# Kernel optimization log

Measured on AMD Instinct MI355X. Metric: run time of the kernel, lower is better.

Reference implementation:

```python
import math
import jax, jax.numpy as jnp
import numpy as np

B, T, D = 2, 1024, 768          # batch, seq, hidden
H = 12                          # attention heads
DH_ATT = D // H
PH, NK, TOPK, DHK = 4, 256, 32, 128  # pkm heads, num product keys, topk, key dim
DQ = PH * DHK * 2               # pkm query projection width
EPS = 1e-5


def _ln(x, g, b):
    m = jnp.mean(x, -1, keepdims=True)
    v = jnp.var(x, -1, keepdims=True)
    return (x - m) * jax.lax.rsqrt(v + EPS) * g + b


def setup_inputs() -> dict:
    key = jax.random.key(0)
    k = jax.random.split(key, 8)
    n = lambda i, s, sc=0.02: jax.random.normal(k[i], s, jnp.float32) * sc
    z = lambda s: jnp.zeros(s, jnp.float32)
    o = lambda s: jnp.ones(s, jnp.float32)
    return {
        "hidden_states": jax.random.normal(k[0], (B, T, D), jnp.float32),
        "wq": n(1, (D, D)), "bq": z((D,)),
        "wk": n(2, (D, D)), "bk": z((D,)),
        "wv": n(3, (D, D)), "bv": z((D,)),
        "wo": n(4, (D, D)), "bo": z((D,)),
        "ln1_g": o((D,)), "ln1_b": z((D,)),
        "ln2_g": o((D,)), "ln2_b": z((D,)),
        "pkm_wq": n(5, (D, DQ)),
        "bn_g": o((DQ,)), "bn_b": z((DQ,)),
        "pkm_keys": n(6, (PH, NK, 2, DHK), 1.0 / math.sqrt(DHK)),
        "pkm_values": n(7, (NK * NK, D), 1.0 / math.sqrt(D)),
    }


def reference(hidden_states, wq, bq, wk, bk, wv, bv, wo, bo,
              ln1_g, ln1_b, ln2_g, ln2_b,
              pkm_wq, bn_g, bn_b, pkm_keys, pkm_values):
    x = hidden_states
    # ---- pre-norm self-attention + residual ----
    h = _ln(x, ln1_g, ln1_b)
    q = (h @ wq + bq).reshape(B, T, H, DH_ATT)
    k = (h @ wk + bk).reshape(B, T, H, DH_ATT)
    v = (h @ wv + bv).reshape(B, T, H, DH_ATT)
    scores = jnp.einsum('bqhd,bkhd->bhqk', q, k) / math.sqrt(DH_ATT)
    probs = jax.nn.softmax(scores, axis=-1)
    attn_out = jnp.einsum('bhqk,bkhd->bqhd', probs, v).reshape(B, T, D) @ wo + bo
    x = x + attn_out
    # ---- pre-norm PKM + residual ----
    h = _ln(x, ln2_g, ln2_b)
    qf = (h @ pkm_wq).reshape(B * T, DQ)
    # BatchNorm1d over tokens (training-mode batch stats)
    mu = jnp.mean(qf, 0)
    var = jnp.var(qf, 0)
    qn = (qf - mu) * jax.lax.rsqrt(var + EPS) * bn_g + bn_b
    # split into the two sub-key query halves: [2, n, PH, DHK]
    qh = jnp.stack(jnp.split(qn, 2, axis=-1)).reshape(2, B * T, PH, DHK)
    # distances against both sub-key codebooks: [n, PH, 2, NK]
    dots = jnp.einsum('pnhd,hkpd->nhpk', qh, pkm_keys)
    s, idx = jax.lax.top_k(dots, TOPK)                       # [n, PH, 2, TOPK]
    all_s = (s[:, :, 0, :, None] + s[:, :, 1, None, :]).reshape(B * T, PH, TOPK * TOPK)
    all_i = (idx[:, :, 0, :, None] * NK + idx[:, :, 1, None, :]).reshape(B * T, PH, TOPK * TOPK)
    fs, fpos = jax.lax.top_k(all_s, TOPK)                    # [n, PH, TOPK]
    vi = jnp.take_along_axis(all_i, fpos, axis=-1)           # cartesian indices
    attn = jax.nn.softmax(fs, axis=-1)
    # EmbeddingBag(mode='sum') with per_sample_weights: gather + weighted sum over PH*TOPK
    pkm_out = jnp.einsum('nhk,nhkd->nd', attn, pkm_values[vi]).reshape(B, T, D)
    return x + pkm_out
```

## Files before the change

kernel.cpp:

```cpp
#include <hip/hip_runtime.h>
#include <hip/hip_bf16.h>

#define B_  2
#define T_  1024
#define D_  768
#define H_  12
#define NT  2048
#define DQ_ 1024
#define PH_ 4
#define NK_ 256
#define TK_ 32
#define DHK_ 128
#define QKVLD 2304
#define CVHALF 25165824L
#define NKEYS (PH_ * NK_ * 2 * DHK_)
#define PREPBLKS 3584

typedef __attribute__((ext_vector_type(8))) short bf16x8;
typedef __attribute__((ext_vector_type(4))) float f32x4;
typedef __attribute__((ext_vector_type(2))) float f32x2;

static __device__ __forceinline__ unsigned short f2bf(float f) {
    union { float f; unsigned u; } c; c.f = f;
    unsigned r = (c.u + 0x7fffu + ((c.u >> 16) & 1u)) >> 16;
    return (unsigned short)r;
}

static __device__ __forceinline__ float bf2f(unsigned short s) {
    union { unsigned u; float f; } c; c.u = ((unsigned)s) << 16;
    return c.f;
}

__global__ __launch_bounds__(256)
void ln_kernel(const float* __restrict__ x, const float* __restrict__ g,
               const float* __restrict__ b, unsigned short* __restrict__ out,
               int nrows,
               const float* __restrict__ wq, const float* __restrict__ wk,
               const float* __restrict__ wv, const float* __restrict__ wo,
               const float* __restrict__ pwq, const float* __restrict__ keys,
               unsigned short* __restrict__ wqkvT, unsigned short* __restrict__ woT,
               unsigned short* __restrict__ pwqT, unsigned short* __restrict__ keyB) {
    int tid = threadIdx.x;
    if ((int)blockIdx.x >= nrows) {
        int tb = blockIdx.x - nrows;
        if (tb >= 3072) {
            long i = ((long)(tb - 3072) * 256 + tid) * 2;
            if (i + 1 < NKEYS + 1) { keyB[i] = f2bf(keys[i]); keyB[i + 1] = f2bf(keys[i + 1]); }
            return;
        }
        __shared__ float t[32][33];
        const float* W; unsigned short* Wt; int N, kx, ny;
        if (tb < 2304) {
            int z = tb / 576, rem = tb % 576;
            kx = rem % 24; ny = rem / 24; N = 768;
            if (z == 0)      { W = wq; Wt = wqkvT; }
            else if (z == 1) { W = wk; Wt = wqkvT + 589824; }
            else if (z == 2) { W = wv; Wt = wqkvT + 2 * 589824; }
            else             { W = wo; Wt = woT; }
        } else {
            int rem = tb - 2304;
            kx = rem % 24; ny = rem / 24; N = 1024;
            W = pwq; Wt = pwqT;
        }
        int k0 = kx * 32, n0 = ny * 32;
        int tx = tid & 31, ty = tid >> 5;
#pragma unroll
        for (int i = 0; i < 4; ++i)
            t[ty + 8 * i][tx] = W[(long)(k0 + ty + 8 * i) * N + n0 + tx];
        __syncthreads();
#pragma unroll
        for (int i = 0; i < 4; ++i)
            Wt[(long)(n0 + ty + 8 * i) * 768 + k0 + tx] = f2bf(t[tx][ty + 8 * i]);
        return;
    }

    int row = blockIdx.x;
    const float* xr = x + (long)row * D_;
    float v0 = xr[tid], v1 = xr[tid + 256], v2 = xr[tid + 512];
    float s = v0 + v1 + v2, ss = v0 * v0 + v1 * v1 + v2 * v2;
#pragma unroll
    for (int o = 1; o < 64; o <<= 1) { s += __shfl_xor(s, o); ss += __shfl_xor(ss, o); }
    __shared__ float ps[4], pss[4];
    int wid = tid >> 6, lane = tid & 63;
    if (lane == 0) { ps[wid] = s; pss[wid] = ss; }
    __syncthreads();
    s = ps[0] + ps[1] + ps[2] + ps[3];
    ss = pss[0] + pss[1] + pss[2] + pss[3];
    float mean = s * (1.f / D_);
    float var = ss * (1.f / D_) - mean * mean;
    float rs = rsqrtf(var + 1e-5f);
    unsigned short* orow = out + (long)row * D_;
    orow[tid]       = f2bf((v0 - mean) * rs * g[tid]       + b[tid]);
    orow[tid + 256] = f2bf((v1 - mean) * rs * g[tid + 256] + b[tid + 256]);
    orow[tid + 512] = f2bf((v2 - mean) * rs * g[tid + 512] + b[tid + 512]);
}

__global__ __launch_bounds__(256)
void gemm_kernel(const unsigned short* __restrict__ A, int lda,
                 const unsigned short* __restrict__ Bt, int ldb,
                 const float* __restrict__ bias,
                 const float* __restrict__ bias2,
                 const float* __restrict__ bias3,
                 const float* __restrict__ res,
                 float* __restrict__ outF,
                 unsigned short* __restrict__ outB,
                 int ldc, int K, int zmode,
                 const float* __restrict__ cvin,
                 unsigned char* __restrict__ cvout,
                 long cvbase, int cvy0) {
    if (cvin && (int)blockIdx.y >= cvy0) {
        long stride = (long)(gridDim.y - cvy0) * gridDim.x * 256 * 8;
        long idx = cvbase +
            ((long)((blockIdx.y - cvy0) * gridDim.x + blockIdx.x) * 256 + threadIdx.x) * 8;
        long end = cvbase + CVHALF;
#pragma unroll 2
        for (; idx < end; idx += stride) {
            f32x4 a = *(const f32x4*)(cvin + idx);
            f32x4 b = *(const f32x4*)(cvin + idx + 4);
            int lo = __builtin_amdgcn_cvt_pk_fp8_f32(a[0], a[1], 0, false);
            lo = __builtin_amdgcn_cvt_pk_fp8_f32(a[2], a[3], lo, true);
            int hi = __builtin_amdgcn_cvt_pk_fp8_f32(b[0], b[1], 0, false);
            hi = __builtin_amdgcn_cvt_pk_fp8_f32(b[2], b[3], hi, true);
            *(uint2*)(cvout + idx) = make_uint2((unsigned)lo, (unsigned)hi);
        }
        return;
    }
    if (zmode == 1) {
        int z = blockIdx.z, ph = z >> 1, half = z & 1;
        A    += half * 512 + ph * 128;
        Bt   += ph * 65536 + half * 128;
        if (outF) outF += ph * 512 + half * 256;
        if (outB) outB += ph * 512 + half * 256;
    }
    const int tid = threadIdx.x;
    const int w = tid >> 6, lane = tid & 63;
    const int ls = lane & 15, g = lane >> 4;
    const int m0 = blockIdx.x * 64, n0 = blockIdx.y * 64;

    __shared__ unsigned short As[64][40];
    __shared__ unsigned short Bs[64][40];

    f32x4 acc[4];
#pragma unroll
    for (int c = 0; c < 4; ++c) acc[c] = (f32x4){0.f, 0.f, 0.f, 0.f};

    const int lrow = tid >> 2, lseg = tid & 3;
    const unsigned short* gA = A + (long)(m0 + lrow) * lda + lseg * 8;
    const unsigned short* gB = Bt + (long)(n0 + lrow) * ldb + lseg * 8;

    for (int kt = 0; kt < K; kt += 32) {
        __syncthreads();
        *(int4*)&As[lrow][lseg * 8] = *(const int4*)(gA + kt);
        *(int4*)&Bs[lrow][lseg * 8] = *(const int4*)(gB + kt);
        __syncthreads();
        bf16x8 bfr = *(const bf16x8*)&Bs[w * 16 + ls][g * 8];
#pragma unroll
        for (int c = 0; c < 4; ++c) {
            bf16x8 afr = *(const bf16x8*)&As[c * 16 + ls][g * 8];
            acc[c] = __builtin_amdgcn_mfma_f32_16x16x32_bf16(afr, bfr, acc[c], 0, 0, 0);
        }
    }
#pragma unroll
    for (int c = 0; c < 4; ++c) {
#pragma unroll
        for (int r = 0; r < 4; ++r) {
            int row = m0 + c * 16 + g * 4 + r;
            int col = n0 + w * 16 + ls;
            float v = acc[c][r];
            if (bias) {
                const float* bp = bias; int cc = col;
                if (zmode == 2) {
                    int sel = col >= 1536 ? 2 : (col >= 768 ? 1 : 0);
                    bp = sel == 0 ? bias : (sel == 1 ? bias2 : bias3);
                    cc = col - sel * 768;
                }
                v += bp[cc];
            }
            long off = (long)row * ldc + col;
            if (res)  v += res[off];
            if (outF) outF[off] = v;
            if (outB) outB[off] = f2bf(v);
        }
    }
}

__global__ __launch_bounds__(512)
void attn_mfma_kernel(const unsigned short* __restrict__ qkv,
                      unsigned short* __restrict__ outg) {
    int bh = blockIdx.x, bb = bh / H_, hh = bh % H_;
    int q0 = blockIdx.y * 128;
    int tid = threadIdx.x, wv = tid >> 6, lane = tid & 63;
    int ls = lane & 15, g = lane >> 4;

    __shared__ unsigned short Klds[128 * 64];
    __shared__ unsigned short Vlds[64 * 128];
    __shared__ unsigned short Plds[8][16 * 128];

    const unsigned short* qrow = qkv + (long)(bb * T_ + q0 + wv * 16 + ls) * QKVLD + hh * 64 + g * 8;
    bf16x8 qf0 = *(const bf16x8*)qrow;
    bf16x8 qf1 = *(const bf16x8*)(qrow + 32);

    f32x4 o_acc[4];
#pragma unroll
    for (int nf = 0; nf < 4; ++nf) o_acc[nf] = (f32x4){0.f, 0.f, 0.f, 0.f};
    float mrun[4] = {-1e30f, -1e30f, -1e30f, -1e30f};
    float lrun[4] = {0.f, 0.f, 0.f, 0.f};

    char* pbase = (char*)&Plds[wv][0];
    const bool doK = tid < 256;
    const int t2 = tid & 255;
    const int d0 = (t2 & 7) * 8, kvq = t2 >> 3;

    bf16x8 streg[4];
    auto loadKV = [&](int kvb) {
        if (doK) {
#pragma unroll
            for (int i = 0; i < 4; ++i) {
                int c = t2 + i * 256;
                streg[i] = *(const bf16x8*)(qkv + (long)(bb * T_ + kvb + (c >> 3)) * QKVLD + 768 + hh * 64 + (c & 7) * 8);
            }
        } else {
            const unsigned short* vb = qkv + (long)(bb * T_ + kvb + kvq * 4) * QKVLD + 1536 + hh * 64 + d0;
#pragma unroll
            for (int i = 0; i < 4; ++i) streg[i] = *(const bf16x8*)(vb + i * QKVLD);
        }
    };

    loadKV(0);
    for (int kt = 0; kt < T_ / 128; ++kt) {
        __syncthreads();
        if (doK) {
#pragma unroll
            for (int i = 0; i < 4; ++i) {
                int c = t2 + i * 256;
                int kv = c >> 3, dc = c & 7;
                *(bf16x8*)((char*)Klds + ((kv * 128 + dc * 16) ^ ((kv & 7) << 4))) = streg[i];
            }
        } else {
#pragma unroll
            for (int j = 0; j < 8; ++j) {
                unsigned lo = (unsigned)(unsigned short)streg[0][j] | ((unsigned)(unsigned short)streg[1][j] << 16);
                unsigned hi = (unsigned)(unsigned short)streg[2][j] | ((unsigned)(unsigned short)streg[3][j] << 16);
                int d = d0 + j;
                *(uint2*)((char*)Vlds + ((d * 256 + kvq * 8) ^ ((d & 7) << 4))) = make_uint2(lo, hi);
            }
        }
        __syncthreads();
        if (kt + 1 < T_ / 128) loadKV((kt + 1) * 128);

        f32x4 sa[8];
#pragma unroll
        for (int f = 0; f < 8; ++f) sa[f] = (f32x4){0.f, 0.f, 0.f, 0.f};
        __builtin_amdgcn_s_setprio(1);
#pragma unroll
        for (int f = 0; f < 8; ++f) {
            int kv = f * 16 + ls;
            bf16x8 b0 = *(const bf16x8*)((char*)Klds + ((kv * 128 + g * 16) ^ ((kv & 7) << 4)));
            bf16x8 b1 = *(const bf16x8*)((char*)Klds + ((kv * 128 + 64 + g * 16) ^ ((kv & 7) << 4)));
            sa[f] = __builtin_amdgcn_mfma_f32_16x16x32_bf16(qf0, b0, sa[f], 0, 0, 0);
            sa[f] = __builtin_amdgcn_mfma_f32_16x16x32_bf16(qf1, b1, sa[f], 0, 0, 0);
        }
        __builtin_amdgcn_s_setprio(0);

        float pw[8][4];
#pragma unroll
        for (int f = 0; f < 8; ++f)
#pragma unroll
            for (int r = 0; r < 4; ++r) pw[f][r] = sa[f][r] * 0.125f;
#pragma unroll
        for (int r = 0; r < 4; ++r) {
            float m = pw[0][r];
#pragma unroll
            for (int f = 1; f < 8; ++f) m = fmaxf(m, pw[f][r]);
            m = fmaxf(m, __shfl_xor(m, 1));
            m = fmaxf(m, __shfl_xor(m, 2));
            m = fmaxf(m, __shfl_xor(m, 4));
            m = fmaxf(m, __shfl_xor(m, 8));
            if (m > mrun[r] + 8.f) {
                float fac = __expf(mrun[r] - m);
                lrun[r] *= fac;
#pragma unroll
                for (int nf = 0; nf < 4; ++nf) o_acc[nf][r] *= fac;
                mrun[r] = m;
            }
            float s = 0.f;
#pragma unroll
            for (int f = 0; f < 8; ++f) { float e = __expf(pw[f][r] - mrun[r]); pw[f][r] = e; s += e; }
            s += __shfl_xor(s, 1); s += __shfl_xor(s, 2);
            s += __shfl_xor(s, 4); s += __shfl_xor(s, 8);
            lrun[r] += s;
        }

#pragma unroll
        for (int f = 0; f < 8; ++f)
#pragma unroll
            for (int r = 0; r < 4; ++r) {
                int qr = g * 4 + r, col = ls + 16 * f;
                *(unsigned short*)(pbase + ((qr * 256 + col * 2) ^ ((qr & 7) << 4))) = f2bf(pw[f][r]);
            }

        __builtin_amdgcn_s_setprio(1);
#pragma unroll
        for (int ks = 0; ks < 4; ++ks) {
            bf16x8 pa = *(const bf16x8*)(pbase + ((ls * 256 + ks * 64 + g * 16) ^ ((ls & 7) << 4)));
#pragma unroll
            for (int nf = 0; nf < 4; ++nf) {
                int d = nf * 16 + ls;
                bf16x8 bv = *(const bf16x8*)((char*)Vlds + ((d * 256 + ks * 64 + g * 16) ^ ((d & 7) << 4)));
                o_acc[nf] = __builtin_amdgcn_mfma_f32_16x16x32_bf16(pa, bv, o_acc[nf], 0, 0, 0);
            }
        }
        __builtin_amdgcn_s_setprio(0);
    }

    float inv[4];
#pragma unroll
    for (int r = 0; r < 4; ++r) inv[r] = 1.f / lrun[r];
#pragma unroll
    for (int nf = 0; nf < 4; ++nf)
#pragma unroll
        for (int r = 0; r < 4; ++r) {
            long row = bb * T_ + q0 + wv * 16 + g * 4 + r;
            outg[row * D_ + hh * 64 + nf * 16 + ls] = f2bf(o_acc[nf][r] * inv[r]);
        }
}

__global__ __launch_bounds__(256)
void bn_part(const unsigned short* __restrict__ qf, float* __restrict__ pS, float* __restrict__ pSS) {
    int c = blockIdx.y * 256 + threadIdx.x;
    int r0 = blockIdx.x * 32;
    float s = 0.f, ss = 0.f;
#pragma unroll 4
    for (int r = 0; r < 32; ++r) {
        float v = bf2f(qf[(long)(r0 + r) * DQ_ + c]);
        s += v; ss += v * v;
    }
    pS[(long)blockIdx.x * DQ_ + c] = s;
    pSS[(long)blockIdx.x * DQ_ + c] = ss;
}

__global__ __launch_bounds__(256)
void qnf_kernel(const unsigned short* __restrict__ qf, const float* __restrict__ pS,
                const float* __restrict__ pSS, const float* __restrict__ g,
                const float* __restrict__ b, unsigned short* __restrict__ qn) {
    int c = blockIdx.y * 256 + threadIdx.x;
    float s = 0.f, ss = 0.f;
#pragma unroll 8
    for (int i = 0; i < 64; ++i) { s += pS[(long)i * DQ_ + c]; ss += pSS[(long)i * DQ_ + c]; }
    float m = s * (1.f / NT);
    float rs = rsqrtf(ss * (1.f / NT) - m * m + 1e-5f);
    float gg = g[c] * rs;
    float bb = b[c] - m * gg;
    int r0 = blockIdx.x * 32;
#pragma unroll 4
    for (int r = 0; r < 32; ++r) {
        long o = (long)(r0 + r) * DQ_ + c;
        qn[o] = f2bf(bf2f(qf[o]) * gg + bb);
    }
}

__global__ __launch_bounds__(256)
void topk_kernel(const unsigned short* __restrict__ dots, float* __restrict__ fs, int* __restrict__ vi) {
    static const unsigned short tab[128] = {
        0,1,2,3,4,5,6,7,8,9,10,11,12,13,14,15,16,17,18,19,20,21,22,23,24,25,26,27,28,29,30,31,
        32,33,34,35,36,37,38,39,40,41,42,43,44,45,46,47,
        64,65,66,67,68,69,70,71,72,73,
        96,97,98,99,100,101,102,103,
        128,129,130,131,132,133,
        160,161,162,163,164,
        192,193,194,195,
        224,225,226,227,
        256,257,258,
        288,289,290,
        320,321, 352,353, 384,385, 416,417, 448,449, 480,481,
        512,544,576,608,640,672,704,736,768,800,832,864,896,928,960,992,
        0xFFFF,0xFFFF,0xFFFF,0xFFFF,0xFFFF,0xFFFF,0xFFFF,0xFFFF,0xFFFF
    };
    __shared__ float sv[2][64];
    __shared__ int   sidx[2][64];
    int tid = threadIdx.x, wv = tid >> 6, lane = tid & 63;
    int slot = wv >> 1, half = wv & 1;
    long task = (long)blockIdx.x * 2 + slot;
    const unsigned short* d = dots + (task >> 2) * 2048 + (task & 3) * 512 + half * 256;

    float v0 = bf2f(d[lane]), v1 = bf2f(d[lane + 64]);
    float v2 = bf2f(d[lane + 128]), v3 = bf2f(d[lane + 192]);
#pragma unroll 1
    for (int t = 0; t < 32; ++t) {
        float bm = v0; int ba = 0;
        if (v1 > bm) { bm = v1; ba = 1; }
        if (v2 > bm) { bm = v2; ba = 2; }
        if (v3 > bm) { bm = v3; ba = 3; }
        float wm = bm;
#pragma unroll
        for (int o = 32; o >= 1; o >>= 1) wm = fmaxf(wm, __shfl_xor(wm, o));
        unsigned long long msk = __ballot(bm == wm);
        int owner = (int)__builtin_ctzll(msk);
        if (lane == owner) {
            sv[slot][half * 32 + t] = wm;
            sidx[slot][half * 32 + t] = ba * 64 + lane;
            if (ba == 0) v0 = -1e30f;
            else if (ba == 1) v1 = -1e30f;
            else if (ba == 2) v2 = -1e30f;
            else v3 = -1e30f;
        }
    }
    __syncthreads();
    if (half) return;

    unsigned short t0 = tab[lane], t1 = tab[lane + 64];
    float c0 = -1e30f, c1 = -1e30f;
    int id0 = 0, id1 = 0;
    {
        int i = t0 >> 5, j = t0 & 31;
        c0 = sv[slot][i] + sv[slot][32 + j];
        id0 = sidx[slot][i] * NK_ + sidx[slot][32 + j];
    }
    if (t1 != 0xFFFF) {
        int i = t1 >> 5, j = t1 & 31;
        c1 = sv[slot][i] + sv[slot][32 + j];
        id1 = sidx[slot][i] * NK_ + sidx[slot][32 + j];
    }

    float* fo = fs + task * 32;
    int*   vo = vi + task * 32;
#pragma unroll 1
    for (int t = 0; t < 32; ++t) {
        float bm = c0; int sel = 0;
        if (c1 > bm) { bm = c1; sel = 1; }
        float wm = bm;
#pragma unroll
        for (int o = 32; o >= 1; o >>= 1) wm = fmaxf(wm, __shfl_xor(wm, o));
        unsigned long long msk = __ballot(bm == wm);
        int owner = (int)__builtin_ctzll(msk);
        if (lane == owner) {
            fo[t] = wm;
            vo[t] = sel ? id1 : id0;
            if (sel) c1 = -1e30f; else c0 = -1e30f;
        }
    }
}

__global__ __launch_bounds__(384)
void pkm_out_fp8(const float* __restrict__ fs, const int* __restrict__ vi,
                 const unsigned char* __restrict__ vals8, const float* __restrict__ x1,
                 float* __restrict__ outp) {
    int n = blockIdx.x, tid = threadIdx.x;
    __shared__ float w[128];
    __shared__ int   rows[128];
    __shared__ float red[3 * 768];
    if (tid < 128) {
        float e = fs[(long)n * 128 + tid];
        rows[tid] = vi[(long)n * 128 + tid];
        float m = e;
#pragma unroll
        for (int o = 16; o >= 1; o >>= 1) m = fmaxf(m, __shfl_xor(m, o));
        float ex = __expf(e - m);
        float s = ex;
#pragma unroll
        for (int o = 16; o >= 1; o >>= 1) s += __shfl_xor(s, o);
        w[tid] = ex / s;
    }
    __syncthreads();
    int slot = tid / 96, chunk = tid % 96;
    float a0=0.f,a1=0.f,a2=0.f,a3=0.f,a4=0.f,a5=0.f,a6=0.f,a7=0.f;
#pragma unroll 4
    for (int e = 0; e < 32; ++e) {
        int er = e * 4 + slot;
        float wgt = w[er];
        long ro = (long)rows[er] * D_;
        uint2 v = *(const uint2*)(vals8 + ro + chunk * 8);
        f32x2 f0 = __builtin_amdgcn_cvt_pk_f32_fp8((int)v.x, false);
        f32x2 f1 = __builtin_amdgcn_cvt_pk_f32_fp8((int)v.x, true);
        f32x2 f2 = __builtin_amdgcn_cvt_pk_f32_fp8((int)v.y, false);
        f32x2 f3 = __builtin_amdgcn_cvt_pk_f32_fp8((int)v.y, true);
        a0 += wgt * f0[0]; a1 += wgt * f0[1]; a2 += wgt * f1[0]; a3 += wgt * f1[1];
        a4 += wgt * f2[0]; a5 += wgt * f2[1]; a6 += wgt * f3[0]; a7 += wgt * f3[1];
    }
    if (slot > 0) {
        float* rp = &red[(slot - 1) * 768 + chunk * 8];
        rp[0]=a0; rp[1]=a1; rp[2]=a2; rp[3]=a3; rp[4]=a4; rp[5]=a5; rp[6]=a6; rp[7]=a7;
    }
    __syncthreads();
    if (slot == 0) {
        long o = (long)n * D_ + chunk * 8;
        const float* r0 = &red[chunk * 8];
        const float* r1 = &red[768 + chunk * 8];
        const float* r2 = &red[1536 + chunk * 8];
        f32x4 xa = *(const f32x4*)(x1 + o);
        f32x4 xb = *(const f32x4*)(x1 + o + 4);
        f32x4 o1 = { a0 + r0[0] + r1[0] + r2[0] + xa[0], a1 + r0[1] + r1[1] + r2[1] + xa[1],
                     a2 + r0[2] + r1[2] + r2[2] + xa[2], a3 + r0[3] + r1[3] + r2[3] + xa[3] };
        f32x4 o2 = { a4 + r0[4] + r1[4] + r2[4] + xb[0], a5 + r0[5] + r1[5] + r2[5] + xb[1],
                     a6 + r0[6] + r1[6] + r2[6] + xb[2], a7 + r0[7] + r1[7] + r2[7] + xb[3] };
        *(f32x4*)(outp + o) = o1;
        *(f32x4*)(outp + o + 4) = o2;
    }
}

__global__ __launch_bounds__(384)
void pkm_out_f32(const float* __restrict__ fs, const int* __restrict__ vi,
                 const float* __restrict__ values, const float* __restrict__ x1,
                 float* __restrict__ outp) {
    int n = blockIdx.x, tid = threadIdx.x;
    __shared__ float w[128];
    __shared__ int   rows[128];
    __shared__ float red[768];
    if (tid < 128) {
        float e = fs[(long)n * 128 + tid];
        rows[tid] = vi[(long)n * 128 + tid];
        float m = e;
#pragma unroll
        for (int o = 16; o >= 1; o >>= 1) m = fmaxf(m, __shfl_xor(m, o));
        float ex = __expf(e - m);
        float s = ex;
#pragma unroll
        for (int o = 16; o >= 1; o >>= 1) s += __shfl_xor(s, o);
        w[tid] = ex / s;
    }
    __syncthreads();
    int slot = tid / 192, chunk = tid % 192;
    float a0 = 0.f, a1 = 0.f, a2 = 0.f, a3 = 0.f;
#pragma unroll 4
    for (int e = 0; e < 64; ++e) {
        int er = e * 2 + slot;
        float wgt = w[er];
        long ro = (long)rows[er] * D_;
        f32x4 v = *(const f32x4*)(values + ro + chunk * 4);
        a0 += wgt * v[0]; a1 += wgt * v[1]; a2 += wgt * v[2]; a3 += wgt * v[3];
    }
    if (slot == 1) {
        f32x4 t = {a0, a1, a2, a3};
        *(f32x4*)&red[chunk * 4] = t;
    }
    __syncthreads();
    if (slot == 0) {
        f32x4 o = *(const f32x4*)&red[chunk * 4];
        f32x4 xr = *(const f32x4*)(x1 + (long)n * D_ + chunk * 4);
        o[0] += a0 + xr[0]; o[1] += a1 + xr[1]; o[2] += a2 + xr[2]; o[3] += a3 + xr[3];
        *(f32x4*)(outp + (long)n * D_ + chunk * 4) = o;
    }
}

extern "C" void kernel_launch(void* const* d_in, const int* in_sizes, int n_in,
                              void* d_out, int out_size, void* d_ws, size_t ws_size,
                              hipStream_t stream) {
    const float* x    = (const float*)d_in[0];
    const float* wq   = (const float*)d_in[1];
    const float* bq   = (const float*)d_in[2];
    const float* wk   = (const float*)d_in[3];
    const float* bk   = (const float*)d_in[4];
    const float* wv   = (const float*)d_in[5];
    const float* bv   = (const float*)d_in[6];
    const float* wo   = (const float*)d_in[7];
    const float* bo   = (const float*)d_in[8];
    const float* ln1g = (const float*)d_in[9];
    const float* ln1b = (const float*)d_in[10];
    const float* ln2g = (const float*)d_in[11];
    const float* ln2b = (const float*)d_in[12];
    const float* pwq  = (const float*)d_in[13];
    const float* bng  = (const float*)d_in[14];
    const float* bnb  = (const float*)d_in[15];
    const float* keys = (const float*)d_in[16];
    const float* vals = (const float*)d_in[17];
    float* out = (float*)d_out;

    char* p = (char*)d_ws;
    auto alloc = [&](size_t bytes) -> char* {
        char* r = p; p += (bytes + 255) & ~(size_t)255; return r;
    };
    unsigned short* wqkvT = (unsigned short*)alloc((size_t)3 * D_ * D_ * 2);
    unsigned short* woT   = (unsigned short*)alloc((size_t)D_ * D_ * 2);
    unsigned short* pwqT  = (unsigned short*)alloc((size_t)D_ * DQ_ * 2);
    unsigned short* keyB  = (unsigned short*)alloc((size_t)NKEYS * 2);
    unsigned short* h1    = (unsigned short*)alloc((size_t)NT * D_ * 2);
    unsigned short* qkvB  = (unsigned short*)alloc((size_t)NT * QKVLD * 2);
    unsigned short* aout  = (unsigned short*)alloc((size_t)NT * D_ * 2);
    float* x1             = (float*)alloc((size_t)NT * D_ * 4);
    unsigned short* h2    = (unsigned short*)alloc((size_t)NT * D_ * 2);
    unsigned short* qfB   = (unsigned short*)alloc((size_t)NT * DQ_ * 2);
    float* pS             = (float*)alloc((size_t)64 * DQ_ * 4);
    float* pSS            = (float*)alloc((size_t)64 * DQ_ * 4);
    unsigned short* qnB   = (unsigned short*)alloc((size_t)NT * DQ_ * 2);
    unsigned short* dots  = (unsigned short*)alloc((size_t)NT * 2048 * 2);
    float* fsb            = (float*)alloc((size_t)NT * PH_ * 32 * 4);
    int*   vib            = (int*)alloc((size_t)NT * PH_ * 32 * 4);

    size_t used = (size_t)(p - (char*)d_ws);
    size_t vbytes = (size_t)NK_ * NK_ * D_;
    bool useTab = (used + vbytes + 256) <= ws_size;
    unsigned char* vals8 = nullptr;
    if (useTab) vals8 = (unsigned char*)alloc(vbytes);

    ln_kernel<<<NT + PREPBLKS, 256, 0, stream>>>(
        x, ln1g, ln1b, h1, NT, wq, wk, wv, wo, pwq, keys, wqkvT, woT, pwqT, keyB);
    gemm_kernel<<<dim3(32, useTab ? 52 : 36), 256, 0, stream>>>(
        h1, D_, wqkvT, D_, bq, bk, bv, nullptr, nullptr, qkvB, QKVLD, D_, 2,
        useTab ? vals : nullptr, vals8, 0L, 36);
    attn_mfma_kernel<<<dim3(B_ * H_, T_ / 128), 512, 0, stream>>>(qkvB, aout);
    gemm_kernel<<<dim3(32, 12), 256, 0, stream>>>(
        aout, D_, woT, D_, bo, nullptr, nullptr, x, x1, nullptr, D_, D_, 0,
        nullptr, nullptr, 0L, 0);
    ln_kernel<<<NT, 256, 0, stream>>>(
        x1, ln2g, ln2b, h2, NT, nullptr, nullptr, nullptr, nullptr, nullptr, nullptr,
        nullptr, nullptr, nullptr, nullptr);
    gemm_kernel<<<dim3(32, useTab ? 32 : 16), 256, 0, stream>>>(
        h2, D_, pwqT, D_, nullptr, nullptr, nullptr, nullptr, nullptr, qfB, DQ_, D_, 0,
        useTab ? vals : nullptr, vals8, CVHALF, 16);
    bn_part<<<dim3(64, 4), 256, 0, stream>>>(qfB, pS, pSS);
    qnf_kernel<<<dim3(64, 4), 256, 0, stream>>>(qfB, pS, pSS, bng, bnb, qnB);
    gemm_kernel<<<dim3(32, 4, 8), 256, 0, stream>>>(
        qnB, DQ_, keyB, 256, nullptr, nullptr, nullptr, nullptr, nullptr, dots, 2048, DHK_, 1,
        nullptr, nullptr, 0L, 0);
    topk_kernel<<<(NT * PH_) / 2, 256, 0, stream>>>(dots, fsb, vib);
    if (useTab)
        pkm_out_fp8<<<NT, 384, 0, stream>>>(fsb, vib, vals8, x1, out);
    else
        pkm_out_f32<<<NT, 384, 0, stream>>>(fsb, vib, vals, x1, out);
}
```

Measured before the change: 259.2 us.

## Fuse PKM top-k into the fp8 gather kernel and add a dedicated dots GEMM

The two-stage product-key top-k selection now runs inside the fp8 value gather/reduce kernel, one 512-thread block per token. Scores and indices stay in shared memory instead of passing through global buffers, and one kernel launch is removed. The key-dot product gets its own kernel that loads the full K=128 tile into LDS at once and issues all MFMAs without a K loop. The cost is a larger block, more shared memory per block and lower occupancy for the gather phase, and a quarter of the threads sit idle during the gather.

```diff
diff --git a/kernel.cpp b/kernel.cpp
--- a/kernel.cpp
+++ b/kernel.cpp
@@ -30,6 +30,22 @@
     union { unsigned u; float f; } c; c.u = ((unsigned)s) << 16;
     return c.f;
 }
+
+__device__ __constant__ unsigned short ctab[128] = {
+    0,1,2,3,4,5,6,7,8,9,10,11,12,13,14,15,16,17,18,19,20,21,22,23,24,25,26,27,28,29,30,31,
+    32,33,34,35,36,37,38,39,40,41,42,43,44,45,46,47,
+    64,65,66,67,68,69,70,71,72,73,
+    96,97,98,99,100,101,102,103,
+    128,129,130,131,132,133,
+    160,161,162,163,164,
+    192,193,194,195,
+    224,225,226,227,
+    256,257,258,
+    288,289,290,
+    320,321, 352,353, 384,385, 416,417, 448,449, 480,481,
+    512,544,576,608,640,672,704,736,768,800,832,864,896,928,960,992,
+    0xFFFF,0xFFFF,0xFFFF,0xFFFF,0xFFFF,0xFFFF,0xFFFF,0xFFFF,0xFFFF
+};
 
 __global__ __launch_bounds__(256)
 void ln_kernel(const float* __restrict__ x, const float* __restrict__ g,
@@ -125,13 +141,6 @@
         }
         return;
     }
-    if (zmode == 1) {
-        int z = blockIdx.z, ph = z >> 1, half = z & 1;
-        A    += half * 512 + ph * 128;
-        Bt   += ph * 65536 + half * 128;
-        if (outF) outF += ph * 512 + half * 256;
-        if (outB) outB += ph * 512 + half * 256;
-    }
     const int tid = threadIdx.x;
     const int w = tid >> 6, lane = tid & 63;
     const int ls = lane & 15, g = lane >> 4;
@@ -182,6 +191,51 @@
             if (outB) outB[off] = f2bf(v);
         }
     }
+}
+
+__global__ __launch_bounds__(256)
+void dots_kernel(const unsigned short* __restrict__ A,
+                 const unsigned short* __restrict__ Bt,
+                 unsigned short* __restrict__ outB) {
+    int z = blockIdx.z, ph = z >> 1, half = z & 1;
+    A    += half * 512 + ph * 128;
+    Bt   += ph * 65536 + half * 128;
+    outB += ph * 512 + half * 256;
+    const int tid = threadIdx.x;
+    const int w = tid >> 6, lane = tid & 63;
+    const int ls = lane & 15, g = lane >> 4;
+    const int m0 = blockIdx.x * 64, n0 = blockIdx.y * 64;
+
+    __shared__ unsigned short As[64][136];
+    __shared__ unsigned short Bs[64][136];
+
+    const int row = tid >> 2, cs = (tid & 3) * 32;
+    const unsigned short* gA = A + (long)(m0 + row) * DQ_ + cs;
+    const unsigned short* gB = Bt + (long)(n0 + row) * 256 + cs;
+#pragma unroll
+    for (int j = 0; j < 4; ++j) {
+        *(int4*)&As[row][cs + 8 * j] = *(const int4*)(gA + 8 * j);
+        *(int4*)&Bs[row][cs + 8 * j] = *(const int4*)(gB + 8 * j);
+    }
+    __syncthreads();
+
+    f32x4 acc[4];
+#pragma unroll
+    for (int c = 0; c < 4; ++c) acc[c] = (f32x4){0.f, 0.f, 0.f, 0.f};
+#pragma unroll
+    for (int kk = 0; kk < 4; ++kk) {
+        bf16x8 bfr = *(const bf16x8*)&Bs[w * 16 + ls][g * 8 + 32 * kk];
+#pragma unroll
+        for (int c = 0; c < 4; ++c) {
+            bf16x8 afr = *(const bf16x8*)&As[c * 16 + ls][g * 8 + 32 * kk];
+            acc[c] = __builtin_amdgcn_mfma_f32_16x16x32_bf16(afr, bfr, acc[c], 0, 0, 0);
+        }
+    }
+#pragma unroll
+    for (int c = 0; c < 4; ++c)
+#pragma unroll
+        for (int r = 0; r < 4; ++r)
+            outB[(long)(m0 + c * 16 + g * 4 + r) * 2048 + n0 + w * 16 + ls] = f2bf(acc[c][r]);
 }
 
 __global__ __launch_bounds__(512)
@@ -359,99 +413,81 @@
     }
 }
 
-__global__ __launch_bounds__(256)
-void topk_kernel(const unsigned short* __restrict__ dots, float* __restrict__ fs, int* __restrict__ vi) {
-    static const unsigned short tab[128] = {
-        0,1,2,3,4,5,6,7,8,9,10,11,12,13,14,15,16,17,18,19,20,21,22,23,24,25,26,27,28,29,30,31,
-        32,33,34,35,36,37,38,39,40,41,42,43,44,45,46,47,
-        64,65,66,67,68,69,70,71,72,73,
-        96,97,98,99,100,101,102,103,
-        128,129,130,131,132,133,
-        160,161,162,163,164,
-        192,193,194,195,
-        224,225,226,227,
-        256,257,258,
-        288,289,290,
-        320,321, 352,353, 384,385, 416,417, 448,449, 480,481,
-        512,544,576,608,640,672,704,736,768,800,832,864,896,928,960,992,
-        0xFFFF,0xFFFF,0xFFFF,0xFFFF,0xFFFF,0xFFFF,0xFFFF,0xFFFF,0xFFFF
-    };
-    __shared__ float sv[2][64];
-    __shared__ int   sidx[2][64];
-    int tid = threadIdx.x, wv = tid >> 6, lane = tid & 63;
-    int slot = wv >> 1, half = wv & 1;
-    long task = (long)blockIdx.x * 2 + slot;
-    const unsigned short* d = dots + (task >> 2) * 2048 + (task & 3) * 512 + half * 256;
-
-    float v0 = bf2f(d[lane]), v1 = bf2f(d[lane + 64]);
-    float v2 = bf2f(d[lane + 128]), v3 = bf2f(d[lane + 192]);
-#pragma unroll 1
-    for (int t = 0; t < 32; ++t) {
-        float bm = v0; int ba = 0;
-        if (v1 > bm) { bm = v1; ba = 1; }
-        if (v2 > bm) { bm = v2; ba = 2; }
-        if (v3 > bm) { bm = v3; ba = 3; }
-        float wm = bm;
-#pragma unroll
-        for (int o = 32; o >= 1; o >>= 1) wm = fmaxf(wm, __shfl_xor(wm, o));
-        unsigned long long msk = __ballot(bm == wm);
-        int owner = (int)__builtin_ctzll(msk);
-        if (lane == owner) {
-            sv[slot][half * 32 + t] = wm;
-            sidx[slot][half * 32 + t] = ba * 64 + lane;
-            if (ba == 0) v0 = -1e30f;
-            else if (ba == 1) v1 = -1e30f;
-            else if (ba == 2) v2 = -1e30f;
-            else v3 = -1e30f;
-        }
-    }
-    __syncthreads();
-    if (half) return;
-
-    unsigned short t0 = tab[lane], t1 = tab[lane + 64];
-    float c0 = -1e30f, c1 = -1e30f;
-    int id0 = 0, id1 = 0;
-    {
-        int i = t0 >> 5, j = t0 & 31;
-        c0 = sv[slot][i] + sv[slot][32 + j];
-        id0 = sidx[slot][i] * NK_ + sidx[slot][32 + j];
-    }
-    if (t1 != 0xFFFF) {
-        int i = t1 >> 5, j = t1 & 31;
-        c1 = sv[slot][i] + sv[slot][32 + j];
-        id1 = sidx[slot][i] * NK_ + sidx[slot][32 + j];
-    }
-
-    float* fo = fs + task * 32;
-    int*   vo = vi + task * 32;
-#pragma unroll 1
-    for (int t = 0; t < 32; ++t) {
-        float bm = c0; int sel = 0;
-        if (c1 > bm) { bm = c1; sel = 1; }
-        float wm = bm;
-#pragma unroll
-        for (int o = 32; o >= 1; o >>= 1) wm = fmaxf(wm, __shfl_xor(wm, o));
-        unsigned long long msk = __ballot(bm == wm);
-        int owner = (int)__builtin_ctzll(msk);
-        if (lane == owner) {
-            fo[t] = wm;
-            vo[t] = sel ? id1 : id0;
-            if (sel) c1 = -1e30f; else c0 = -1e30f;
-        }
-    }
-}
-
-__global__ __launch_bounds__(384)
-void pkm_out_fp8(const float* __restrict__ fs, const int* __restrict__ vi,
-                 const unsigned char* __restrict__ vals8, const float* __restrict__ x1,
-                 float* __restrict__ outp) {
-    int n = blockIdx.x, tid = threadIdx.x;
+__global__ __launch_bounds__(512)
+void pkm_tail_fp8(const unsigned short* __restrict__ dots,
+                  const unsigned char* __restrict__ vals8,
+                  const float* __restrict__ x1,
+                  float* __restrict__ outp) {
+    __shared__ float sv[4][64];
+    __shared__ int   sidx[4][64];
     __shared__ float w[128];
     __shared__ int   rows[128];
     __shared__ float red[3 * 768];
+    int n = blockIdx.x, tid = threadIdx.x;
+    int wv = tid >> 6, lane = tid & 63;
+    int slot = wv >> 1, half = wv & 1;
+
+    {
+        const unsigned short* d = dots + (long)n * 2048 + slot * 512 + half * 256;
+        float v0 = bf2f(d[lane]), v1 = bf2f(d[lane + 64]);
+        float v2 = bf2f(d[lane + 128]), v3 = bf2f(d[lane + 192]);
+#pragma unroll 1
+        for (int t = 0; t < 32; ++t) {
+            float bm = v0; int ba = 0;
+            if (v1 > bm) { bm = v1; ba = 1; }
+            if (v2 > bm) { bm = v2; ba = 2; }
+            if (v3 > bm) { bm = v3; ba = 3; }
+            float wm = bm;
+#pragma unroll
+            for (int o = 32; o >= 1; o >>= 1) wm = fmaxf(wm, __shfl_xor(wm, o));
+            unsigned long long msk = __ballot(bm == wm);
+            int owner = (int)__builtin_ctzll(msk);
+            if (lane == owner) {
+                sv[slot][half * 32 + t] = wm;
+                sidx[slot][half * 32 + t] = ba * 64 + lane;
+                if (ba == 0) v0 = -1e30f;
+                else if (ba == 1) v1 = -1e30f;
+                else if (ba == 2) v2 = -1e30f;
+                else v3 = -1e30f;
+            }
+        }
+    }
+    __syncthreads();
+
+    if (!half) {
+        unsigned short t0 = ctab[lane], t1 = ctab[lane + 64];
+        float c0 = -1e30f, c1 = -1e30f;
+        int id0 = 0, id1 = 0;
+        {
+            int i = t0 >> 5, j = t0 & 31;
+            c0 = sv[slot][i] + sv[slot][32 + j];
+            id0 = sidx[slot][i] * NK_ + sidx[slot][32 + j];
+        }
+        if (t1 != 0xFFFF) {
+            int i = t1 >> 5, j = t1 & 31;
+            c1 = sv[slot][i] + sv[slot][32 + j];
+            id1 = sidx[slot][i] * NK_ + sidx[slot][32 + j];
+        }
+#pragma unroll 1
+        for (int t = 0; t < 32; ++t) {
+            float bm = c0; int sel = 0;
+            if (c1 > bm) { bm = c1; sel = 1; }
+            float wm = bm;
+#pragma unroll
+            for (int o = 32; o >= 1; o >>= 1) wm = fmaxf(wm, __shfl_xor(wm, o));
+            unsigned long long msk = __ballot(bm == wm);
+            int owner = (int)__builtin_ctzll(msk);
+            if (lane == owner) {
+                w[slot * 32 + t] = wm;
+                rows[slot * 32 + t] = sel ? id1 : id0;
+                if (sel) c1 = -1e30f; else c0 = -1e30f;
+            }
+        }
+    }
+    __syncthreads();
+
     if (tid < 128) {
-        float e = fs[(long)n * 128 + tid];
-        rows[tid] = vi[(long)n * 128 + tid];
+        float e = w[tid];
         float m = e;
 #pragma unroll
         for (int o = 16; o >= 1; o >>= 1) m = fmaxf(m, __shfl_xor(m, o));
@@ -462,27 +498,30 @@
         w[tid] = ex / s;
     }
     __syncthreads();
-    int slot = tid / 96, chunk = tid % 96;
+
+    int gs = tid >> 7, chunk = tid & 127;
     float a0=0.f,a1=0.f,a2=0.f,a3=0.f,a4=0.f,a5=0.f,a6=0.f,a7=0.f;
+    if (chunk < 96) {
 #pragma unroll 4
-    for (int e = 0; e < 32; ++e) {
-        int er = e * 4 + slot;
-        float wgt = w[er];
-        long ro = (long)rows[er] * D_;
-        uint2 v = *(const uint2*)(vals8 + ro + chunk * 8);
-        f32x2 f0 = __builtin_amdgcn_cvt_pk_f32_fp8((int)v.x, false);
-        f32x2 f1 = __builtin_amdgcn_cvt_pk_f32_fp8((int)v.x, true);
-        f32x2 f2 = __builtin_amdgcn_cvt_pk_f32_fp8((int)v.y, false);
-        f32x2 f3 = __builtin_amdgcn_cvt_pk_f32_fp8((int)v.y, true);
-        a0 += wgt * f0[0]; a1 += wgt * f0[1]; a2 += wgt * f1[0]; a3 += wgt * f1[1];
-        a4 += wgt * f2[0]; a5 += wgt * f2[1]; a6 += wgt * f3[0]; a7 += wgt * f3[1];
-    }
-    if (slot > 0) {
-        float* rp = &red[(slot - 1) * 768 + chunk * 8];
-        rp[0]=a0; rp[1]=a1; rp[2]=a2; rp[3]=a3; rp[4]=a4; rp[5]=a5; rp[6]=a6; rp[7]=a7;
-    }
-    __syncthreads();
-    if (slot == 0) {
+        for (int e = 0; e < 32; ++e) {
+            int er = e * 4 + gs;
+            float wgt = w[er];
+            long ro = (long)rows[er] * D_;
+            uint2 v = *(const uint2*)(vals8 + ro + chunk * 8);
+            f32x2 f0 = __builtin_amdgcn_cvt_pk_f32_fp8((int)v.x, false);
+            f32x2 f1 = __builtin_amdgcn_cvt_pk_f32_fp8((int)v.x, true);
+            f32x2 f2 = __builtin_amdgcn_cvt_pk_f32_fp8((int)v.y, false);
+            f32x2 f3 = __builtin_amdgcn_cvt_pk_f32_fp8((int)v.y, true);
+            a0 += wgt * f0[0]; a1 += wgt * f0[1]; a2 += wgt * f1[0]; a3 += wgt * f1[1];
+            a4 += wgt * f2[0]; a5 += wgt * f2[1]; a6 += wgt * f3[0]; a7 += wgt * f3[1];
+        }
+        if (gs > 0) {
+            float* rp = &red[(gs - 1) * 768 + chunk * 8];
+            rp[0]=a0; rp[1]=a1; rp[2]=a2; rp[3]=a3; rp[4]=a4; rp[5]=a5; rp[6]=a6; rp[7]=a7;
+        }
+    }
+    __syncthreads();
+    if (gs == 0 && chunk < 96) {
         long o = (long)n * D_ + chunk * 8;
         const float* r0 = &red[chunk * 8];
         const float* r1 = &red[768 + chunk * 8];
@@ -495,6 +534,73 @@
                      a6 + r0[6] + r1[6] + r2[6] + xb[2], a7 + r0[7] + r1[7] + r2[7] + xb[3] };
         *(f32x4*)(outp + o) = o1;
         *(f32x4*)(outp + o + 4) = o2;
+    }
+}
+
+__global__ __launch_bounds__(256)
+void topk_kernel(const unsigned short* __restrict__ dots, float* __restrict__ fs, int* __restrict__ vi) {
+    __shared__ float sv[2][64];
+    __shared__ int   sidx[2][64];
+    int tid = threadIdx.x, wv = tid >> 6, lane = tid & 63;
+    int slot = wv >> 1, half = wv & 1;
+    long task = (long)blockIdx.x * 2 + slot;
+    const unsigned short* d = dots + (task >> 2) * 2048 + (task & 3) * 512 + half * 256;
+
+    float v0 = bf2f(d[lane]), v1 = bf2f(d[lane + 64]);
+    float v2 = bf2f(d[lane + 128]), v3 = bf2f(d[lane + 192]);
+#pragma unroll 1
+    for (int t = 0; t < 32; ++t) {
+        float bm = v0; int ba = 0;
+        if (v1 > bm) { bm = v1; ba = 1; }
+        if (v2 > bm) { bm = v2; ba = 2; }
+        if (v3 > bm) { bm = v3; ba = 3; }
+        float wm = bm;
+#pragma unroll
+        for (int o = 32; o >= 1; o >>= 1) wm = fmaxf(wm, __shfl_xor(wm, o));
+        unsigned long long msk = __ballot(bm == wm);
+        int owner = (int)__builtin_ctzll(msk);
+        if (lane == owner) {
+            sv[slot][half * 32 + t] = wm;
+            sidx[slot][half * 32 + t] = ba * 64 + lane;
+            if (ba == 0) v0 = -1e30f;
+            else if (ba == 1) v1 = -1e30f;
+            else if (ba == 2) v2 = -1e30f;
+            else v3 = -1e30f;
+        }
+    }
+    __syncthreads();
+    if (half) return;
+
+    unsigned short t0 = ctab[lane], t1 = ctab[lane + 64];
+    float c0 = -1e30f, c1 = -1e30f;
+    int id0 = 0, id1 = 0;
+    {
+        int i = t0 >> 5, j = t0 & 31;
+        c0 = sv[slot][i] + sv[slot][32 + j];
+        id0 = sidx[slot][i] * NK_ + sidx[slot][32 + j];
+    }
+    if (t1 != 0xFFFF) {
+        int i = t1 >> 5, j = t1 & 31;
+        c1 = sv[slot][i] + sv[slot][32 + j];
+        id1 = sidx[slot][i] * NK_ + sidx[slot][32 + j];
+    }
+
+    float* fo = fs + task * 32;
+    int*   vo = vi + task * 32;
+#pragma unroll 1
+    for (int t = 0; t < 32; ++t) {
+        float bm = c0; int sel = 0;
+        if (c1 > bm) { bm = c1; sel = 1; }
+        float wm = bm;
+#pragma unroll
+        for (int o = 32; o >= 1; o >>= 1) wm = fmaxf(wm, __shfl_xor(wm, o));
+        unsigned long long msk = __ballot(bm == wm);
+        int owner = (int)__builtin_ctzll(msk);
+        if (lane == owner) {
+            fo[t] = wm;
+            vo[t] = sel ? id1 : id0;
+            if (sel) c1 = -1e30f; else c0 = -1e30f;
+        }
     }
 }
 
@@ -609,12 +715,11 @@
         useTab ? vals : nullptr, vals8, CVHALF, 16);
     bn_part<<<dim3(64, 4), 256, 0, stream>>>(qfB, pS, pSS);
     qnf_kernel<<<dim3(64, 4), 256, 0, stream>>>(qfB, pS, pSS, bng, bnb, qnB);
-    gemm_kernel<<<dim3(32, 4, 8), 256, 0, stream>>>(
-        qnB, DQ_, keyB, 256, nullptr, nullptr, nullptr, nullptr, nullptr, dots, 2048, DHK_, 1,
-        nullptr, nullptr, 0L, 0);
-    topk_kernel<<<(NT * PH_) / 2, 256, 0, stream>>>(dots, fsb, vib);
-    if (useTab)
-        pkm_out_fp8<<<NT, 384, 0, stream>>>(fsb, vib, vals8, x1, out);
-    else
+    dots_kernel<<<dim3(32, 4, 8), 256, 0, stream>>>(qnB, keyB, dots);
+    if (useTab) {
+        pkm_tail_fp8<<<NT, 512, 0, stream>>>(dots, vals8, x1, out);
+    } else {
+        topk_kernel<<<(NT * PH_) / 2, 256, 0, stream>>>(dots, fsb, vib);
         pkm_out_f32<<<NT, 384, 0, stream>>>(fsb, vib, vals, x1, out);
-}
+    }
+}
```

Measured after the change: 243.9 us. 1.06x faster.
